# Optimization experiments

Measured on AMD Instinct MI355X. Metric: run time of the kernel, lower is better.

The kernel has to match this reference:

```python
import jax, jax.numpy as jnp
import numpy as np

B, N, CIN, CK, M0 = 2, 4096, 64, 64, 64
NS = 16  # nsample; split into NS//2 cosine + NS//2 euclidean neighbors
LEAKY = 0.1


def _leaky(x):
    return jax.nn.leaky_relu(x, LEAKY)


def _knn_cosine(k, xyz, new_xyz):
    # xyz [B,M,C], new_xyz [B,S,C] -> idx [B,S,k] of smallest cosine distance
    s = new_xyz / jnp.sqrt(jnp.sum(new_xyz ** 2, -1, keepdims=True) + 1e-8)
    d = xyz / jnp.sqrt(jnp.sum(xyz ** 2, -1, keepdims=True) + 1e-8)
    dist = 1.0 - jnp.einsum('bsc,bmc->bsm', s, d)
    return jax.lax.top_k(-dist, k)[1]


def _knn_euclid(k, xyz, new_xyz):
    # squared euclidean distance [B,S,M]
    dist = (jnp.sum(new_xyz ** 2, -1)[:, :, None]
            + jnp.sum(xyz ** 2, -1)[:, None, :]
            - 2.0 * jnp.einsum('bsc,bmc->bsm', new_xyz, xyz))
    return jax.lax.top_k(-dist, k)[1]


def _group(points, idx):
    # points [B,M,C], idx [B,S,K] -> [B,S,K,C]
    return jax.vmap(lambda p, i: p[i])(points, idx)


def _cross(xyz1, xyz2, p1, p2, k1, k2, W_pos, b_pos, W_m1, b_m1, W_m2, b_m2):
    # all point tensors channel-first [B,C,N]; transpose to [B,N,C]
    xyz1t = xyz1.transpose(0, 2, 1)
    xyz2t = xyz2.transpose(0, 2, 1)
    p1t = p1.transpose(0, 2, 1)
    p2t = p2.transpose(0, 2, 1)
    k1t = k1.transpose(0, 2, 1)
    k2t = k2.transpose(0, 2, 1)
    kh = NS // 2
    idx_c = _knn_cosine(kh, k2t, k1t)      # [B,N1,kh] feature-space KNN
    idx_p = _knn_euclid(kh, xyz2t, xyz1t)  # [B,N1,kh] xyz-space KNN
    neighbor_xyz = jnp.concatenate([_group(xyz2t, idx_c), _group(xyz2t, idx_p)], axis=2)  # [B,N1,NS,3]
    direction = neighbor_xyz - xyz1t[:, :, None, :]
    g2 = jnp.concatenate([_group(p2t, idx_c), _group(p2t, idx_p)], axis=2)  # [B,N1,NS,D]
    pos = jnp.einsum('bnkc,dc->bnkd', direction, W_pos) + b_pos  # 1x1 conv on xyz offsets
    new = _leaky(g2 + p1t[:, :, None, :] + pos)  # fused add + leaky relu (bn=Identity)
    new = _leaky(jnp.einsum('bnkd,ed->bnke', new, W_m1) + b_m1)
    new = _leaky(jnp.einsum('bnkd,ed->bnke', new, W_m2) + b_m2)
    new = jnp.max(new, axis=2)  # max-pool over neighbor dim -> [B,N1,D]
    return new.transpose(0, 2, 1)  # [B,D,N1]


def setup_inputs() -> dict:
    key = jax.random.key(0)
    ks = jax.random.split(key, 12)
    rn = lambda k, shape, s=1.0: jax.random.normal(k, shape, jnp.float32) * s
    return {
        'pc1': rn(ks[0], (B, 3, N)),
        'pc2': rn(ks[1], (B, 3, N)),
        'feat1': rn(ks[2], (B, CIN, N)),
        'feat2': rn(ks[3], (B, CIN, N)),
        'knn1': rn(ks[4], (B, CK, N)),
        'knn2': rn(ks[5], (B, CK, N)),
        'W_t11': rn(ks[6], (M0, CIN), 0.1),
        'b_t11': jnp.zeros((M0,), jnp.float32),
        'W_t22': rn(ks[7], (M0, CIN), 0.1),
        'b_t22': jnp.zeros((M0,), jnp.float32),
        'W_pos': rn(ks[8], (M0, 3), 0.1),
        'b_pos': jnp.zeros((M0,), jnp.float32),
        'W_m1': rn(ks[9], (M0, M0), 0.1),
        'b_m1': jnp.zeros((M0,), jnp.float32),
        'W_m2': rn(ks[10], (M0, M0), 0.1),
        'b_m2': jnp.zeros((M0,), jnp.float32),
    }


def reference(pc1, pc2, feat1, feat2, knn1, knn2,
              W_t11, b_t11, W_t22, b_t22, W_pos, b_pos,
              W_m1, b_m1, W_m2, b_m2):
    # cross_t11 / cross_t22: 1x1 Conv1d in_channel -> mlp[0]
    f1a = jnp.einsum('dc,bcn->bdn', W_t11, feat1) + b_t11[None, :, None]
    f2a = jnp.einsum('dc,bcn->bdn', W_t22, feat2) + b_t22[None, :, None]
    f2b = jnp.einsum('dc,bcn->bdn', W_t11, feat2) + b_t11[None, :, None]
    f1b = jnp.einsum('dc,bcn->bdn', W_t22, feat1) + b_t22[None, :, None]
    feat1_new = _cross(pc1, pc2, f1a, f2a, knn1, knn2, W_pos, b_pos, W_m1, b_m1, W_m2, b_m2)
    feat2_new = _cross(pc2, pc1, f2b, f1b, knn2, knn1, W_pos, b_pos, W_m1, b_m1, W_m2, b_m2)
    return (feat1_new, feat2_new)
```

## Files before the change

kernel.cpp:

```cpp
#include <hip/hip_runtime.h>
#include <hip/hip_bf16.h>

#define BB 2
#define NN 4096
#define CH 64

typedef __bf16 bf16x8 __attribute__((ext_vector_type(8)));
typedef float f32x4 __attribute__((ext_vector_type(4)));

__device__ __forceinline__ float lrelu(float v) { return fmaxf(v, 0.1f * v); }
__device__ __forceinline__ float tobf(const __hip_bfloat16& h) { return __bfloat162float(h); }

#define PC1_C 0
#define PC2_C 24576
#define F1_C 49152
#define F2_C 573440
#define K1_C 1097728
#define K2_C 1622016
#define WT11_C 2146304
#define BT11_C 2150400
#define WT22_C 2150464
#define BT22_C 2154560
#define WPOS_C 2154624
#define BPOS_C 2154816
#define WM1_C 2154880
#define BM1_C 2158976
#define WM2_C 2159040
#define BM2_C 2163136
#define CN_TOTAL 2163200

__device__ __forceinline__ unsigned fmap(float s) {
  unsigned u = __float_as_uint(s);
  return u ^ ((unsigned)((int)u >> 31) | 0x80000000u);
}

__device__ __forceinline__ unsigned umaxu(unsigned a, unsigned b) { return a > b ? a : b; }
__device__ __forceinline__ void casu(unsigned& a, unsigned& b) {
  unsigned mx = a > b ? a : b;
  unsigned mn = a > b ? b : a;
  a = mx; b = mn;
}

__device__ __forceinline__ void bitonic8(unsigned bd[8]) {
  casu(bd[0], bd[4]); casu(bd[1], bd[5]); casu(bd[2], bd[6]); casu(bd[3], bd[7]);
  casu(bd[0], bd[2]); casu(bd[1], bd[3]); casu(bd[4], bd[6]); casu(bd[5], bd[7]);
  casu(bd[0], bd[1]); casu(bd[2], bd[3]); casu(bd[4], bd[5]); casu(bd[6], bd[7]);
}

__device__ __forceinline__ void merge4(unsigned bd[8], unsigned k0, unsigned k1,
                                       unsigned k2, unsigned k3) {
  casu(k0, k1); casu(k2, k3); casu(k0, k2); casu(k1, k3); casu(k1, k2);
  bd[4] = umaxu(bd[4], k3); bd[5] = umaxu(bd[5], k2);
  bd[6] = umaxu(bd[6], k1); bd[7] = umaxu(bd[7], k0);
  bitonic8(bd);
}

__device__ __forceinline__ void merge88(unsigned a[8], const unsigned b[8]) {
  a[0] = umaxu(a[0], b[7]); a[1] = umaxu(a[1], b[6]);
  a[2] = umaxu(a[2], b[5]); a[3] = umaxu(a[3], b[4]);
  a[4] = umaxu(a[4], b[3]); a[5] = umaxu(a[5], b[2]);
  a[6] = umaxu(a[6], b[1]); a[7] = umaxu(a[7], b[0]);
  bitonic8(a);
}

__global__ void k_detect(const unsigned short* __restrict__ pc1raw, int* __restrict__ flag) {
  int lane = threadIdx.x;
  int bad = 0;
#pragma unroll
  for (int i = 0; i < 64; ++i) {
    unsigned short u = pc1raw[lane * 64 + i];
    int e = (u >> 7) & 0xFF;
    bad += (e >= 140) ? 1 : 0;
  }
#pragma unroll
  for (int s = 32; s; s >>= 1) bad += __shfl_xor(bad, s, 64);
  if (lane == 0) *flag = (bad > 16) ? 1 : 0;
}

__global__ __launch_bounds__(256) void k_ingest(
    const void* p0, const void* p1, const void* p2, const void* p3,
    const void* p4, const void* p5, const void* p6, const void* p7,
    const void* p8, const void* p9, const void* p10, const void* p11,
    const void* p12, const void* p13, const void* p14, const void* p15,
    const int* __restrict__ flag, float* __restrict__ dst) {
  const int cum[17] = {0, 24576, 49152, 573440, 1097728, 1622016, 2146304, 2150400,
                       2150464, 2154560, 2154624, 2154816, 2154880, 2158976, 2159040,
                       2163136, 2163200};
  size_t t = (size_t)blockIdx.x * 256 + threadIdx.x;
  if (t >= (size_t)CN_TOTAL) return;
  int seg = 0;
#pragma unroll
  for (int i = 1; i < 16; ++i) seg += (t >= (size_t)cum[i]) ? 1 : 0;
  size_t local = t - (size_t)cum[seg];
  const void* ptrs[16] = {p0, p1, p2, p3, p4, p5, p6, p7, p8, p9, p10, p11, p12, p13, p14, p15};
  const void* p = ptrs[seg];
  float v;
  if (*flag) v = ((const float*)p)[local];
  else       v = tobf(((const __hip_bfloat16*)p)[local]);
  if (!(v == v) || fabsf(v) > 1e30f) v = 0.f;
  dst[t] = v;
}

__global__ __launch_bounds__(256) void k_prep_misc(const float* __restrict__ cn,
                                                   __hip_bfloat16* __restrict__ wmb,
                                                   float4* __restrict__ xyzt,
                                                   float4* __restrict__ wp4) {
  int bid = blockIdx.x;
  if (bid < 32) {
    int t = bid * 256 + threadIdx.x;
    float v = (t < 4096) ? cn[WM1_C + t] : cn[WM2_C + (t - 4096)];
    wmb[t] = __float2bfloat16(v);
  } else if (bid < 96) {
    int t = (bid - 32) * 256 + threadIdx.x;
    int n = t & (NN - 1);
    int b = (t >> 12) & 1;
    int a = t >> 13;
    const float* p = cn + (a ? PC2_C : PC1_C) + (size_t)b * 3 * NN + n;
    float x = p[0], y = p[NN], z = p[2 * NN];
    xyzt[(size_t)(a * BB + b) * NN + n] = make_float4(x, y, z, x * x + y * y + z * z);
  } else {
    int c = threadIdx.x;
    if (c < 64)
      wp4[c] = make_float4(cn[WPOS_C + 3 * c], cn[WPOS_C + 3 * c + 1],
                           cn[WPOS_C + 3 * c + 2], cn[BPOS_C + c]);
  }
}

__global__ __launch_bounds__(256) void k_prep_knn(const float* __restrict__ cn,
                                                  float* __restrict__ knnt,
                                                  __hip_bfloat16* __restrict__ knnb) {
  int t = blockIdx.x * 256 + threadIdx.x;
  int n = t & (NN - 1);
  int b = (t >> 12) & 1;
  int a = t >> 13;
  const float* col = cn + (a ? K2_C : K1_C) + (size_t)b * CH * NN + n;
  float s = 0.f;
#pragma unroll
  for (int c = 0; c < CH; ++c) { float v = col[(size_t)c * NN]; s += v * v; }
  float inv = 1.0f / sqrtf(s + 1e-8f);
  size_t row = (size_t)(a * BB + b) * NN + n;
  float* o = knnt + row * CH;
  __hip_bfloat16* ob = knnb + row * CH;
#pragma unroll
  for (int c = 0; c < CH; ++c) {
    float v = col[(size_t)c * NN] * inv;
    o[c] = v;
    ob[c] = __float2bfloat16(v);
  }
}

__global__ __launch_bounds__(256) void k_conv(const float* __restrict__ cn,
                                              float* __restrict__ fbuf) {
  __shared__ float wl[CH * CH];
  int bid = blockIdx.x;
  int tile = bid & (NN / 4 - 1);
  int b = (bid >> 10) & 1;
  int sel = bid >> 11;
  const float* W = cn + ((sel == 0 || sel == 2) ? WT11_C : WT22_C);
  const float* bias = cn + ((sel == 0 || sel == 2) ? BT11_C : BT22_C);
  const float* feat = cn + ((sel == 0 || sel == 3) ? F1_C : F2_C);
  int t = threadIdx.x;
#pragma unroll
  for (int i = 0; i < 16; ++i) {
    int e = t * 16 + i;
    wl[(e & 63) * 64 + (e >> 6)] = W[e];
  }
  __syncthreads();
  int p = t >> 6, d = t & 63;
  int n = tile * 4 + p;
  const float* fc = feat + (size_t)b * CH * NN + n;
  float acc = bias[d];
#pragma unroll
  for (int c = 0; c < CH; ++c) acc += wl[c * 64 + d] * fc[(size_t)c * NN];
  fbuf[((size_t)(sel * BB + b) * NN + n) * CH + d] = acc;
}

__global__ __launch_bounds__(512, 4) void k_knn4(const __hip_bfloat16* __restrict__ knnb,
                                                 const float* __restrict__ knnt,
                                                 const float4* __restrict__ xyzt,
                                                 int* __restrict__ idxf) {
  __shared__ unsigned sk[16 * 8 * 33];
  __shared__ int cidx[16 * 16];
  int bid = blockIdx.x;
  int qt = bid & (NN / 16 - 1);
  int b = (bid >> 8) & 1;
  int x = bid >> 9;
  int w = threadIdx.x >> 6;
  int lane = threadIdx.x & 63;
  int lo = lane & 15, g = lane >> 4;
  int q0 = qt * 16;
  int j0 = w * (NN / 8);
  int ss = w * 4 + g;
  int hw = lane >> 5, sl = lane & 31;
  int qq = w * 2 + hw;
  size_t qbase = (size_t)(x * BB + b) * NN;
  size_t dbase = (size_t)((1 - x) * BB + b) * NN;

  const __hip_bfloat16* qb = knnb + (qbase + q0) * CH;
  bf16x8 qf0 = *reinterpret_cast<const bf16x8*>(qb + lo * CH + g * 8);
  bf16x8 qf1 = *reinterpret_cast<const bf16x8*>(qb + lo * CH + 32 + g * 8);
  const __hip_bfloat16* db = knnb + dbase * CH;
  const float4 q4 = xyzt[qbase + q0 + lo];
  const float4* dbx = xyzt + dbase;
  float tx = 2.f * q4.x, ty = 2.f * q4.y, tz = 2.f * q4.z;

  unsigned bc0[8], bc1[8], be0[8], be1[8];
#pragma unroll
  for (int k = 0; k < 8; ++k) { bc0[k] = 0u; bc1[k] = 0u; be0[k] = 0u; be1[k] = 0u; }

  auto STEP = [&](const bf16x8& A0, const bf16x8& A1, const float4& P0,
                  const float4& P1, const float4& P2, const float4& P3,
                  int rcv, unsigned (&bc)[8], unsigned (&be)[8]) {
    f32x4 acc = {0.f, 0.f, 0.f, 0.f};
    acc = __builtin_amdgcn_mfma_f32_16x16x32_bf16(A0, qf0, acc, 0, 0, 0);
    acc = __builtin_amdgcn_mfma_f32_16x16x32_bf16(A1, qf1, acc, 0, 0, 0);
    float v0 = fmaf(tx, P0.x, fmaf(ty, P0.y, fmaf(tz, P0.z, -P0.w)));
    float v1 = fmaf(tx, P1.x, fmaf(ty, P1.y, fmaf(tz, P1.z, -P1.w)));
    float v2 = fmaf(tx, P2.x, fmaf(ty, P2.y, fmaf(tz, P2.z, -P2.w)));
    float v3 = fmaf(tx, P3.x, fmaf(ty, P3.y, fmaf(tz, P3.z, -P3.w)));
    unsigned r = (unsigned)rcv;
    merge4(bc, (__float_as_uint(acc[0] + 4.0f) & 0xFFFFF000u) | r,
               (__float_as_uint(acc[1] + 4.0f) & 0xFFFFF000u) | (r - 1),
               (__float_as_uint(acc[2] + 4.0f) & 0xFFFFF000u) | (r - 2),
               (__float_as_uint(acc[3] + 4.0f) & 0xFFFFF000u) | (r - 3));
    merge4(be, (fmap(v0) & 0xFFFFF000u) | r,
               (fmap(v1) & 0xFFFFF000u) | (r - 1),
               (fmap(v2) & 0xFFFFF000u) | (r - 2),
               (fmap(v3) & 0xFFFFF000u) | (r - 3));
  };

  const __hip_bfloat16* arA = db + (size_t)(j0 + lo) * CH + g * 8;
  const __hip_bfloat16* arB = arA + 16 * CH;
  const float4* peA = dbx + j0 + g * 4;
  const float4* peB = peA + 16;
  int rc = 4095 - j0 - g * 4;

  bf16x8 aA0 = *reinterpret_cast<const bf16x8*>(arA);
  bf16x8 aA1 = *reinterpret_cast<const bf16x8*>(arA + 32);
  float4 pA0 = peA[0], pA1 = peA[1], pA2 = peA[2], pA3 = peA[3];

  for (int i = 0; i < 15; ++i) {
    bf16x8 aB0 = *reinterpret_cast<const bf16x8*>(arB);
    bf16x8 aB1 = *reinterpret_cast<const bf16x8*>(arB + 32);
    float4 pB0 = peB[0], pB1 = peB[1], pB2 = peB[2], pB3 = peB[3];
    STEP(aA0, aA1, pA0, pA1, pA2, pA3, rc, bc0, be0);
    arA += 32 * CH; peA += 32;
    aA0 = *reinterpret_cast<const bf16x8*>(arA);
    aA1 = *reinterpret_cast<const bf16x8*>(arA + 32);
    pA0 = peA[0]; pA1 = peA[1]; pA2 = peA[2]; pA3 = peA[3];
    STEP(aB0, aB1, pB0, pB1, pB2, pB3, rc - 16, bc1, be1);
    arB += 32 * CH; peB += 32;
    rc -= 32;
  }
  {
    bf16x8 aB0 = *reinterpret_cast<const bf16x8*>(arB);
    bf16x8 aB1 = *reinterpret_cast<const bf16x8*>(arB + 32);
    float4 pB0 = peB[0], pB1 = peB[1], pB2 = peB[2], pB3 = peB[3];
    STEP(aA0, aA1, pA0, pA1, pA2, pA3, rc, bc0, be0);
    STEP(aB0, aB1, pB0, pB1, pB2, pB3, rc - 16, bc1, be1);
  }
  merge88(bc0, bc1);
  merge88(be0, be1);

#pragma unroll
  for (int k = 0; k < 8; ++k) sk[(lo * 8 + k) * 33 + ss] = bc0[k];
  __syncthreads();
  {
    unsigned e[16];
#pragma unroll
    for (int k = 0; k < 8; ++k) e[k] = sk[(qq * 8 + k) * 33 + sl];
#pragma unroll
    for (int k = 8; k < 16; ++k) e[k] = 0u;
#pragma unroll
    for (int s = 1; s < 32; s <<= 1) {
      unsigned f[16];
#pragma unroll
      for (int k = 0; k < 16; ++k) f[k] = (unsigned)__shfl_xor((int)e[k], s, 64);
#pragma unroll
      for (int i = 0; i < 16; ++i) e[i] = umaxu(e[i], f[15 - i]);
      casu(e[0], e[8]); casu(e[1], e[9]); casu(e[2], e[10]); casu(e[3], e[11]);
      casu(e[4], e[12]); casu(e[5], e[13]); casu(e[6], e[14]); casu(e[7], e[15]);
      casu(e[0], e[4]); casu(e[1], e[5]); casu(e[2], e[6]); casu(e[3], e[7]);
      casu(e[8], e[12]); casu(e[9], e[13]); casu(e[10], e[14]); casu(e[11], e[15]);
      casu(e[0], e[2]); casu(e[1], e[3]); casu(e[4], e[6]); casu(e[5], e[7]);
      casu(e[8], e[10]); casu(e[9], e[11]); casu(e[12], e[14]); casu(e[13], e[15]);
      casu(e[0], e[1]); casu(e[2], e[3]); casu(e[4], e[5]); casu(e[6], e[7]);
      casu(e[8], e[9]); casu(e[10], e[11]); casu(e[12], e[13]); casu(e[14], e[15]);
    }
    if (sl == 0) {
#pragma unroll
      for (int k = 0; k < 16; ++k) cidx[qq * 16 + k] = 4095 - (int)(e[k] & 4095u);
    }
    int c = sl >> 1, hr = sl & 1;
    int idx = cidx[qq * 16 + c];
    const float4* qr = reinterpret_cast<const float4*>(knnt + (qbase + q0 + qq) * CH) + hr * 8;
    const float4* dr = reinterpret_cast<const float4*>(knnt + (dbase + idx) * CH) + hr * 8;
    float v = 0.f;
#pragma unroll 4
    for (int cb = 0; cb < 8; ++cb) {
      float4 qv = qr[cb], dv = dr[cb];
      v += qv.x * dv.x + qv.y * dv.y + qv.z * dv.z + qv.w * dv.w;
    }
    v += __shfl_xor(v, 1, 64);
    int ii = idx;
#pragma unroll
    for (int k = 2; k <= 32; k <<= 1) {
#pragma unroll
      for (int j = k >> 1; j >= 1; j >>= 1) {
        float ov = __shfl_xor(v, j, 64);
        int oi = __shfl_xor(ii, j, 64);
        bool ob = (ov > v) || (ov == v && oi < ii);
        bool want = (((sl & k) == 0) == ((sl & j) == 0));
        bool take = (want == ob);
        v = take ? ov : v;
        ii = take ? oi : ii;
      }
    }
    if (sl < 16 && (sl & 1) == 0) idxf[(qbase + q0 + qq) * 16 + (sl >> 1)] = ii;
  }
  __syncthreads();

#pragma unroll
  for (int k = 0; k < 8; ++k) sk[(lo * 8 + k) * 33 + ss] = be0[k];
  __syncthreads();
  {
    unsigned e[16];
#pragma unroll
    for (int k = 0; k < 8; ++k) e[k] = sk[(qq * 8 + k) * 33 + sl];
#pragma unroll
    for (int k = 8; k < 16; ++k) e[k] = 0u;
#pragma unroll
    for (int s = 1; s < 32; s <<= 1) {
      unsigned f[16];
#pragma unroll
      for (int k = 0; k < 16; ++k) f[k] = (unsigned)__shfl_xor((int)e[k], s, 64);
#pragma unroll
      for (int i = 0; i < 16; ++i) e[i] = umaxu(e[i], f[15 - i]);
      casu(e[0], e[8]); casu(e[1], e[9]); casu(e[2], e[10]); casu(e[3], e[11]);
      casu(e[4], e[12]); casu(e[5], e[13]); casu(e[6], e[14]); casu(e[7], e[15]);
      casu(e[0], e[4]); casu(e[1], e[5]); casu(e[2], e[6]); casu(e[3], e[7]);
      casu(e[8], e[12]); casu(e[9], e[13]); casu(e[10], e[14]); casu(e[11], e[15]);
      casu(e[0], e[2]); casu(e[1], e[3]); casu(e[4], e[6]); casu(e[5], e[7]);
      casu(e[8], e[10]); casu(e[9], e[11]); casu(e[12], e[14]); casu(e[13], e[15]);
      casu(e[0], e[1]); casu(e[2], e[3]); casu(e[4], e[5]); casu(e[6], e[7]);
      casu(e[8], e[9]); casu(e[10], e[11]); casu(e[12], e[13]); casu(e[14], e[15]);
    }
    if (sl == 0) {
#pragma unroll
      for (int k = 0; k < 16; ++k) cidx[qq * 16 + k] = 4095 - (int)(e[k] & 4095u);
    }
    int c = sl >> 1;
    int idx = cidx[qq * 16 + c];
    const float4 qx4 = xyzt[qbase + q0 + qq];
    float4 p = xyzt[dbase + idx];
    float v = fmaf(2.f * qx4.x, p.x, fmaf(2.f * qx4.y, p.y, fmaf(2.f * qx4.z, p.z, -p.w)));
    int ii = idx;
#pragma unroll
    for (int k = 2; k <= 32; k <<= 1) {
#pragma unroll
      for (int j = k >> 1; j >= 1; j >>= 1) {
        float ov = __shfl_xor(v, j, 64);
        int oi = __shfl_xor(ii, j, 64);
        bool ob = (ov > v) || (ov == v && oi < ii);
        bool want = (((sl & k) == 0) == ((sl & j) == 0));
        bool take = (want == ob);
        v = take ? ov : v;
        ii = take ? oi : ii;
      }
    }
    if (sl < 16 && (sl & 1) == 0) idxf[(qbase + q0 + qq) * 16 + 8 + (sl >> 1)] = ii;
  }
}

__global__ __launch_bounds__(256) void k_mlp(const float* __restrict__ fbuf,
                                             const float4* __restrict__ xyzt,
                                             const int* __restrict__ idxf,
                                             const float4* __restrict__ wp4,
                                             const __hip_bfloat16* __restrict__ wmb,
                                             const float* __restrict__ cn,
                                             float* __restrict__ out) {
  __shared__ __bf16 h1s[4 * 16 * 72];
  const int t = threadIdx.x;
  const int wv = t >> 6, L = t & 63;
  const int lo = L & 15, g = L >> 4;
  int bid = blockIdx.x;
  const int qt = bid & (NN / 4 - 1);
  const int b = (bid >> 10) & 1;
  const int x = bid >> 11;
  const int q = qt * 4 + wv;

  bf16x8 w1f[4][2], w2f[4][2];
#pragma unroll
  for (int tt = 0; tt < 4; ++tt)
#pragma unroll
    for (int kc = 0; kc < 2; ++kc) {
      int e = tt * 16 + lo, c0 = kc * 32 + g * 8;
      w1f[tt][kc] = *reinterpret_cast<const bf16x8*>(wmb + e * 64 + c0);
      w2f[tt][kc] = *reinterpret_cast<const bf16x8*>(wmb + 4096 + e * 64 + c0);
    }

  const float* pq  = fbuf + ((size_t)((x ? 2 : 0) * BB + b)) * NN * CH;
  const float* pdb = fbuf + ((size_t)((x ? 3 : 1) * BB + b)) * NN * CH;
  const float4* qx  = xyzt + (size_t)(x * BB + b) * NN;
  const float4* dbx = xyzt + (size_t)((1 - x) * BB + b) * NN;

  const int m = lo;
  int jm = idxf[(((size_t)x * BB + b) * NN + q) * 16 + m];
  jm &= (NN - 1);
  const float4 q4 = qx[q];
  const float4 p4 = dbx[jm];
  const float dx = p4.x - q4.x, dy = p4.y - q4.y, dz = p4.z - q4.z;

  const float4* g2v = reinterpret_cast<const float4*>(pdb + (size_t)jm * CH);
  const float4* pqv = reinterpret_cast<const float4*>(pq + (size_t)q * CH);
  float hv[16];
  {
    float4 t0 = g2v[g * 2], t1 = g2v[g * 2 + 1], t2 = g2v[g * 2 + 8], t3 = g2v[g * 2 + 9];
    float4 u0 = pqv[g * 2], u1 = pqv[g * 2 + 1], u2 = pqv[g * 2 + 8], u3 = pqv[g * 2 + 9];
    hv[0] = t0.x + u0.x; hv[1] = t0.y + u0.y; hv[2] = t0.z + u0.z; hv[3] = t0.w + u0.w;
    hv[4] = t1.x + u1.x; hv[5] = t1.y + u1.y; hv[6] = t1.z + u1.z; hv[7] = t1.w + u1.w;
    hv[8] = t2.x + u2.x; hv[9] = t2.y + u2.y; hv[10] = t2.z + u2.z; hv[11] = t2.w + u2.w;
    hv[12] = t3.x + u3.x; hv[13] = t3.y + u3.y; hv[14] = t3.z + u3.z; hv[15] = t3.w + u3.w;
  }

  bf16x8 a0, a1;
#pragma unroll
  for (int kc = 0; kc < 2; ++kc) {
#pragma unroll
    for (int j = 0; j < 8; ++j) {
      int c = kc * 32 + g * 8 + j;
      float4 wp = wp4[c];
      float v = hv[kc * 8 + j] + wp.x * dx + wp.y * dy + wp.z * dz + wp.w;
      v = lrelu(v);
      if (kc == 0) a0[j] = (__bf16)v; else a1[j] = (__bf16)v;
    }
  }

  __bf16* hrow = h1s + wv * 16 * 72;
#pragma unroll
  for (int tt = 0; tt < 4; ++tt) {
    float bv = cn[BM1_C + tt * 16 + lo];
    f32x4 acc = {bv, bv, bv, bv};
    acc = __builtin_amdgcn_mfma_f32_16x16x32_bf16(a0, w1f[tt][0], acc, 0, 0, 0);
    acc = __builtin_amdgcn_mfma_f32_16x16x32_bf16(a1, w1f[tt][1], acc, 0, 0, 0);
#pragma unroll
    for (int r = 0; r < 4; ++r) {
      float v = lrelu(acc[r]);
      hrow[(g * 4 + r) * 72 + tt * 16 + lo] = (__bf16)v;
    }
  }
  __syncthreads();
  bf16x8 h1a = *reinterpret_cast<const bf16x8*>(hrow + m * 72 + g * 8);
  bf16x8 h1b = *reinterpret_cast<const bf16x8*>(hrow + m * 72 + 32 + g * 8);

  size_t obase = ((size_t)(x * BB + b) * CH) * NN;
#pragma unroll
  for (int tt = 0; tt < 4; ++tt) {
    float bv = cn[BM2_C + tt * 16 + lo];
    f32x4 acc = {bv, bv, bv, bv};
    acc = __builtin_amdgcn_mfma_f32_16x16x32_bf16(h1a, w2f[tt][0], acc, 0, 0, 0);
    acc = __builtin_amdgcn_mfma_f32_16x16x32_bf16(h1b, w2f[tt][1], acc, 0, 0, 0);
    float v = fmaxf(fmaxf(lrelu(acc[0]), lrelu(acc[1])), fmaxf(lrelu(acc[2]), lrelu(acc[3])));
    v = fmaxf(v, __shfl_xor(v, 16, 64));
    v = fmaxf(v, __shfl_xor(v, 32, 64));
    if (g == 0) out[obase + (size_t)(tt * 16 + lo) * NN + q] = v;
  }
}

#define CN_OFF 0
#define FB_OFF ((size_t)CN_TOTAL)
#define KT_OFF (FB_OFF + (size_t)4 * BB * NN * CH)
#define XZ_OFF (KT_OFF + (size_t)2 * BB * NN * CH)
#define WP4_OFF (XZ_OFF + (size_t)2 * BB * NN * 4)
#define WMB_OFF (WP4_OFF + 256)
#define IDX_OFF (WMB_OFF + 4096)
#define FLAG_OFF (IDX_OFF + 262144)
#define KNB_OFF (FLAG_OFF + 4)

extern "C" void kernel_launch(void* const* d_in, const int* in_sizes, int n_in,
                              void* d_out, int out_size, void* d_ws, size_t ws_size,
                              hipStream_t stream) {
  float* ws = (float*)d_ws;
  float* cn = ws + CN_OFF;
  int* flag = (int*)(ws + FLAG_OFF);

  k_detect<<<1, 64, 0, stream>>>((const unsigned short*)d_in[0], flag);
  k_ingest<<<(CN_TOTAL + 255) / 256, 256, 0, stream>>>(
      d_in[0], d_in[1], d_in[2], d_in[3], d_in[4], d_in[5], d_in[6], d_in[7],
      d_in[8], d_in[9], d_in[10], d_in[11], d_in[12], d_in[13], d_in[14], d_in[15],
      flag, cn);
  k_prep_misc<<<97, 256, 0, stream>>>(cn, (__hip_bfloat16*)(ws + WMB_OFF),
                                      (float4*)(ws + XZ_OFF), (float4*)(ws + WP4_OFF));
  k_prep_knn<<<(2 * BB * NN) / 256, 256, 0, stream>>>(cn, ws + KT_OFF,
                                                     (__hip_bfloat16*)(ws + KNB_OFF));
  k_conv<<<4 * BB * (NN / 4), 256, 0, stream>>>(cn, ws + FB_OFF);
  k_knn4<<<2 * BB * (NN / 16), 512, 0, stream>>>(
      (const __hip_bfloat16*)(ws + KNB_OFF), ws + KT_OFF,
      (const float4*)(ws + XZ_OFF), (int*)(ws + IDX_OFF));
  k_mlp<<<2 * BB * (NN / 4), 256, 0, stream>>>(ws + FB_OFF, (const float4*)(ws + XZ_OFF),
                                               (const int*)(ws + IDX_OFF), (const float4*)(ws + WP4_OFF),
                                               (const __hip_bfloat16*)(ws + WMB_OFF), cn,
                                               (float*)d_out);
}
```

Measured before the change: 304.4 us.

## Move 1x1 conv projections to bf16 split-precision MFMA with shared feature loads

```diff
diff --git a/kernel.cpp b/kernel.cpp
--- a/kernel.cpp
+++ b/kernel.cpp
@@ -29,6 +29,8 @@
 #define BM2_C 2163136
 #define CN_TOTAL 2163200
 
+#define FHALF (2 * BB * NN * CH)
+
 __device__ __forceinline__ unsigned fmap(float s) {
   unsigned u = __float_as_uint(s);
   return u ^ ((unsigned)((int)u >> 31) | 0x80000000u);
@@ -104,7 +106,8 @@
 __global__ __launch_bounds__(256) void k_prep_misc(const float* __restrict__ cn,
                                                    __hip_bfloat16* __restrict__ wmb,
                                                    float4* __restrict__ xyzt,
-                                                   float4* __restrict__ wp4) {
+                                                   float4* __restrict__ wp4,
+                                                   __hip_bfloat16* __restrict__ wcb) {
   int bid = blockIdx.x;
   if (bid < 32) {
     int t = bid * 256 + threadIdx.x;
@@ -118,11 +121,19 @@
     const float* p = cn + (a ? PC2_C : PC1_C) + (size_t)b * 3 * NN + n;
     float x = p[0], y = p[NN], z = p[2 * NN];
     xyzt[(size_t)(a * BB + b) * NN + n] = make_float4(x, y, z, x * x + y * y + z * z);
-  } else {
+  } else if (bid == 96) {
     int c = threadIdx.x;
     if (c < 64)
       wp4[c] = make_float4(cn[WPOS_C + 3 * c], cn[WPOS_C + 3 * c + 1],
                            cn[WPOS_C + 3 * c + 2], cn[BPOS_C + c]);
+  } else {
+    int t = (bid - 97) * 256 + threadIdx.x;
+    int w = t >> 12, e = t & 4095;
+    float v = cn[(w ? WT22_C : WT11_C) + e];
+    __hip_bfloat16 hi = __float2bfloat16(v);
+    __hip_bfloat16 lo = __float2bfloat16(v - tobf(hi));
+    wcb[w * 4096 + e] = hi;
+    wcb[8192 + w * 4096 + e] = lo;
   }
 }
 
@@ -149,30 +160,65 @@
   }
 }
 
-__global__ __launch_bounds__(256) void k_conv(const float* __restrict__ cn,
-                                              float* __restrict__ fbuf) {
-  __shared__ float wl[CH * CH];
+__global__ __launch_bounds__(256) void k_prep_feat(const float* __restrict__ cn,
+                                                   __hip_bfloat16* __restrict__ fhl) {
+  int t = blockIdx.x * 256 + threadIdx.x;
+  int n = t & (NN - 1);
+  int b = (t >> 12) & 1;
+  int a = t >> 13;
+  const float* col = cn + (a ? F2_C : F1_C) + (size_t)b * CH * NN + n;
+  __hip_bfloat16* oh = fhl + ((size_t)(a * BB + b) * NN + n) * CH;
+  __hip_bfloat16* ol = oh + FHALF;
+#pragma unroll
+  for (int c = 0; c < CH; ++c) {
+    float v = col[(size_t)c * NN];
+    __hip_bfloat16 hi = __float2bfloat16(v);
+    oh[c] = hi;
+    ol[c] = __float2bfloat16(v - tobf(hi));
+  }
+}
+
+__global__ __launch_bounds__(256) void k_conv2(const __hip_bfloat16* __restrict__ fhl,
+                                               const __hip_bfloat16* __restrict__ wcb,
+                                               const float* __restrict__ cn,
+                                               float* __restrict__ fbuf) {
   int bid = blockIdx.x;
-  int tile = bid & (NN / 4 - 1);
-  int b = (bid >> 10) & 1;
-  int sel = bid >> 11;
-  const float* W = cn + ((sel == 0 || sel == 2) ? WT11_C : WT22_C);
-  const float* bias = cn + ((sel == 0 || sel == 2) ? BT11_C : BT22_C);
-  const float* feat = cn + ((sel == 0 || sel == 3) ? F1_C : F2_C);
+  int ntile = bid & 255;
+  int b = (bid >> 8) & 1;
+  int a = bid >> 9;
   int t = threadIdx.x;
-#pragma unroll
-  for (int i = 0; i < 16; ++i) {
-    int e = t * 16 + i;
-    wl[(e & 63) * 64 + (e >> 6)] = W[e];
-  }
-  __syncthreads();
-  int p = t >> 6, d = t & 63;
-  int n = tile * 4 + p;
-  const float* fc = feat + (size_t)b * CH * NN + n;
-  float acc = bias[d];
-#pragma unroll
-  for (int c = 0; c < CH; ++c) acc += wl[c * 64 + d] * fc[(size_t)c * NN];
-  fbuf[((size_t)(sel * BB + b) * NN + n) * CH + d] = acc;
+  int dt = t >> 6;
+  int lane = t & 63;
+  int lo = lane & 15, g = lane >> 4;
+
+  const __hip_bfloat16* fb = fhl + ((size_t)(a * BB + b) * NN + ntile * 16 + lo) * CH;
+  bf16x8 ah0 = *reinterpret_cast<const bf16x8*>(fb + g * 8);
+  bf16x8 ah1 = *reinterpret_cast<const bf16x8*>(fb + 32 + g * 8);
+  bf16x8 al0 = *reinterpret_cast<const bf16x8*>(fb + FHALF + g * 8);
+  bf16x8 al1 = *reinterpret_cast<const bf16x8*>(fb + FHALF + 32 + g * 8);
+
+#pragma unroll
+  for (int w = 0; w < 2; ++w) {
+    const __hip_bfloat16* wb = wcb + w * 4096 + (dt * 16 + lo) * 64;
+    bf16x8 wh0 = *reinterpret_cast<const bf16x8*>(wb + g * 8);
+    bf16x8 wh1 = *reinterpret_cast<const bf16x8*>(wb + 32 + g * 8);
+    bf16x8 wl0 = *reinterpret_cast<const bf16x8*>(wb + 8192 + g * 8);
+    bf16x8 wl1 = *reinterpret_cast<const bf16x8*>(wb + 8192 + 32 + g * 8);
+    float bv = cn[(w ? BT22_C : BT11_C) + dt * 16 + lo];
+    f32x4 acc = {bv, bv, bv, bv};
+    acc = __builtin_amdgcn_mfma_f32_16x16x32_bf16(ah0, wh0, acc, 0, 0, 0);
+    acc = __builtin_amdgcn_mfma_f32_16x16x32_bf16(ah1, wh1, acc, 0, 0, 0);
+    acc = __builtin_amdgcn_mfma_f32_16x16x32_bf16(al0, wh0, acc, 0, 0, 0);
+    acc = __builtin_amdgcn_mfma_f32_16x16x32_bf16(al1, wh1, acc, 0, 0, 0);
+    acc = __builtin_amdgcn_mfma_f32_16x16x32_bf16(ah0, wl0, acc, 0, 0, 0);
+    acc = __builtin_amdgcn_mfma_f32_16x16x32_bf16(ah1, wl1, acc, 0, 0, 0);
+    int sel = a ? (w ? 1 : 2) : (w ? 3 : 0);
+    float* ob = fbuf + ((size_t)(sel * BB + b) * NN + ntile * 16 + g * 4) * CH + dt * 16 + lo;
+    ob[0 * CH] = acc[0];
+    ob[1 * CH] = acc[1];
+    ob[2 * CH] = acc[2];
+    ob[3 * CH] = acc[3];
+  }
 }
 
 __global__ __launch_bounds__(512, 4) void k_knn4(const __hip_bfloat16* __restrict__ knnb,
@@ -476,6 +522,8 @@
 #define IDX_OFF (WMB_OFF + 4096)
 #define FLAG_OFF (IDX_OFF + 262144)
 #define KNB_OFF (FLAG_OFF + 4)
+#define FHL_OFF (KNB_OFF + (size_t)BB * NN * CH)
+#define WCB_OFF (FHL_OFF + (size_t)2 * BB * NN * CH)
 
 extern "C" void kernel_launch(void* const* d_in, const int* in_sizes, int n_in,
                               void* d_out, int out_size, void* d_ws, size_t ws_size,
@@ -489,11 +537,14 @@
       d_in[0], d_in[1], d_in[2], d_in[3], d_in[4], d_in[5], d_in[6], d_in[7],
       d_in[8], d_in[9], d_in[10], d_in[11], d_in[12], d_in[13], d_in[14], d_in[15],
       flag, cn);
-  k_prep_misc<<<97, 256, 0, stream>>>(cn, (__hip_bfloat16*)(ws + WMB_OFF),
-                                      (float4*)(ws + XZ_OFF), (float4*)(ws + WP4_OFF));
+  k_prep_misc<<<129, 256, 0, stream>>>(cn, (__hip_bfloat16*)(ws + WMB_OFF),
+                                       (float4*)(ws + XZ_OFF), (float4*)(ws + WP4_OFF),
+                                       (__hip_bfloat16*)(ws + WCB_OFF));
   k_prep_knn<<<(2 * BB * NN) / 256, 256, 0, stream>>>(cn, ws + KT_OFF,
                                                      (__hip_bfloat16*)(ws + KNB_OFF));
-  k_conv<<<4 * BB * (NN / 4), 256, 0, stream>>>(cn, ws + FB_OFF);
+  k_prep_feat<<<(2 * BB * NN) / 256, 256, 0, stream>>>(cn, (__hip_bfloat16*)(ws + FHL_OFF));
+  k_conv2<<<1024, 256, 0, stream>>>((const __hip_bfloat16*)(ws + FHL_OFF),
+                                    (const __hip_bfloat16*)(ws + WCB_OFF), cn, ws + FB_OFF);
   k_knn4<<<2 * BB * (NN / 16), 512, 0, stream>>>(
       (const __hip_bfloat16*)(ws + KNB_OFF), ws + KT_OFF,
       (const float4*)(ws + XZ_OFF), (int*)(ws + IDX_OFF));
```

Result: faster. 295.5 us (-2.9%).
